# Performance work log

Hardware: AMD Instinct MI355X
Metric: run time of the kernel (lower is better)

Reference implementation:

```python
import jax, jax.numpy as jnp
import numpy as np

B, T, IN, H, OUT = 256, 100, 128, 1024, 35
BITS = 4
SLOPE = 25.0
THR_H = 1.0
THR_O = 1.0
BETA1, BETA2, BETA3, BETA4 = 0.9, 0.85, 0.8, 0.95


def fake_quant(w, w_min, w_max, bits=BITS):
    # FakeQuantize in training mode: STE -> forward value is quantized, grad passes through clamp
    levels = 2 ** bits
    scale = (w_max - w_min) / (levels - 1)
    wc = jnp.clip(w, w_min, w_max)
    q = jnp.round((wc - w_min) / scale) * scale + w_min
    return wc + jax.lax.stop_gradient(q - wc)


@jax.custom_vjp
def spike(x):
    # Heaviside forward, fast-sigmoid surrogate backward (snn.surrogate.fast_sigmoid)
    return (x > 0).astype(x.dtype)

def _spike_fwd(x):
    return (x > 0).astype(x.dtype), x

def _spike_bwd(x, g):
    return (g / (SLOPE * jnp.abs(x) + 1.0) ** 2,)

spike.defvjp(_spike_fwd, _spike_bwd)


def lif_step(cur, mem, beta, thr, reset_mechanism):
    # snntorch Leaky (reset_delay semantics): reset computed from previous mem, detached
    reset = jax.lax.stop_gradient((mem > thr).astype(cur.dtype))
    base = beta * mem + cur
    if reset_mechanism == "subtract":
        mem_new = base - reset * thr
    else:  # "zero"
        mem_new = base - reset * base
    spk = spike(mem_new - thr)
    return spk, mem_new


def setup_inputs() -> dict:
    key = jax.random.key(0)
    ks = jax.random.split(key, 5)
    x = jax.random.normal(ks[0], (B, T, IN), dtype=jnp.float32)
    # QuantLinear init: uniform(w_min, w_max); fc1 uses (-0.5, 0.5), others (0.001, 1.0)
    w1 = jax.random.uniform(ks[1], (H, IN), minval=-0.5, maxval=0.5, dtype=jnp.float32)
    w2 = jax.random.uniform(ks[2], (H, H), minval=0.001, maxval=1.0, dtype=jnp.float32)
    w3 = jax.random.uniform(ks[3], (H, H), minval=0.001, maxval=1.0, dtype=jnp.float32)
    w4 = jax.random.uniform(ks[4], (OUT, H), minval=0.001, maxval=1.0, dtype=jnp.float32)
    return {"x": x, "w1": w1, "w2": w2, "w3": w3, "w4": w4}


def reference(x, w1, w2, w3, w4):
    # hoist weight quantization out of the time loop (identical math each step)
    q1 = fake_quant(w1, -0.5, 0.5)
    q2 = fake_quant(w2, 0.001, 1.0)
    q3 = fake_quant(w3, 0.001, 1.0)
    q4 = fake_quant(w4, 0.001, 1.0)
    xs = jnp.transpose(x, (1, 0, 2)) / 15.0  # [T, B, IN]
    Bx = x.shape[0]

    def step(carry, xt):
        m1, m2, m3, m4 = carry
        s1, m1 = lif_step(xt @ q1.T, m1, BETA1, THR_H, "subtract")
        s2, m2 = lif_step(s1 @ q2.T, m2, BETA2, THR_H, "subtract")
        s3, m3 = lif_step(s2 @ q3.T, m3, BETA3, THR_H, "subtract")
        s4, m4 = lif_step(s3 @ q4.T, m4, BETA4, THR_O, "zero")
        return (m1, m2, m3, m4), (s1, s2, s3, s4, m4)

    init = (jnp.zeros((Bx, H), x.dtype), jnp.zeros((Bx, H), x.dtype),
            jnp.zeros((Bx, H), x.dtype), jnp.zeros((Bx, OUT), x.dtype))
    _, (spk1, spk2, spk3, spk4, mem4) = jax.lax.scan(step, init, xs)
    # stacked along time dim 0, matching torch.stack(dim=0)
    return spk1, spk2, spk3, spk4, mem4
```

## Files before the change

### kernel.cpp

```cpp
#include <hip/hip_runtime.h>
#include <stdint.h>

#define NB  256
#define NT  100
#define NIN 128
#define NH  1024
#define NOUT 35

#define O_SPK2 26214400ull
#define O_SPK3 52428800ull
#define O_SPK4 78643200ull
#define O_MEM4 79539200ull

#define WS_XT   0ull
#define WS_Q1T  13107200ull
#define WS_K2T  13631488ull
#define WS_K3T  14680064ull
#define WS_K4T  15728640ull

#define S2C ((float)((1.0 - 0.001) / 15.0))
#define S1C ((float)(1.0 / 15.0))

__global__ __launch_bounds__(256) void k_prep(const float* __restrict__ w1,
                       const float* __restrict__ w2, const float* __restrict__ w3,
                       const float* __restrict__ w4, uint8_t* __restrict__ ws)
{
  const int bid = blockIdx.x, tid = threadIdx.x;
  if (bid < 512) {
    const float* W = (bid < 256) ? w2 : w3;
    uint8_t* K = ws + ((bid < 256) ? WS_K2T : WS_K3T);
    const int tb = bid & 255;
    const int i0 = (tb & 15) << 6, j0 = (tb >> 4) << 6;
    __shared__ uint8_t tile[64 * 68];
    const int jl = tid >> 4, iq = (tid & 15) << 2;
    #pragma unroll
    for (int k = 0; k < 4; ++k) {
      const int jloc = jl + k * 16;
      const float4 v = *(const float4*)&W[(size_t)(j0 + jloc) * 1024 + i0 + iq];
      float wc;
      wc = fminf(fmaxf(v.x, 0.001f), 1.0f); tile[(iq + 0) * 68 + jloc] = (uint8_t)(int)rintf((wc - 0.001f) / S2C);
      wc = fminf(fmaxf(v.y, 0.001f), 1.0f); tile[(iq + 1) * 68 + jloc] = (uint8_t)(int)rintf((wc - 0.001f) / S2C);
      wc = fminf(fmaxf(v.z, 0.001f), 1.0f); tile[(iq + 2) * 68 + jloc] = (uint8_t)(int)rintf((wc - 0.001f) / S2C);
      wc = fminf(fmaxf(v.w, 0.001f), 1.0f); tile[(iq + 3) * 68 + jloc] = (uint8_t)(int)rintf((wc - 0.001f) / S2C);
    }
    __syncthreads();
    const int li = tid >> 2, cq = tid & 3;
    const uint32_t* tp = (const uint32_t*)&tile[li * 68 + (cq << 4)];
    *(uint4*)&K[(size_t)(i0 + li) * 1024 + j0 + (cq << 4)] =
        make_uint4(tp[0], tp[1], tp[2], tp[3]);
    return;
  }
  long long id = (long long)(bid - 512) * 256 + tid;
  if (id < 49152) {
    int i = (int)(id / 48), j = (int)(id % 48);
    uint8_t v = 0;
    if (j < NOUT) {
      float wv = w4[(size_t)j * 1024 + i];
      float wc = fminf(fmaxf(wv, 0.001f), 1.0f);
      v = (uint8_t)(int)rintf((wc - 0.001f) / S2C);
    }
    ws[WS_K4T + id] = v;
    return;
  }
  id -= 49152;
  if (id < 131072) {
    int i = (int)(id >> 10), j = (int)(id & 1023);
    float wv = w1[(size_t)j * 128 + i];
    float wc = fminf(fmaxf(wv, -0.5f), 0.5f);
    float q = rintf((wc + 0.5f) / S1C) * S1C - 0.5f;
    ((float*)(ws + WS_Q1T))[id] = q;
  }
}

__global__ __launch_bounds__(512, 1) void k_spk1(const float* __restrict__ x,
                                                 const float* __restrict__ q1T,
                                                 float* __restrict__ out)
{
  const int b = blockIdx.x;
  const int tid = threadIdx.x;
  const int lane = tid & 63;
  const float* xb = x + (size_t)b * NT * NIN;
  float m1a = 0.f, m1b = 0.f;

  for (int c = 0; c < 4; ++c) {
    float xv0[25], xv1[25];
    #pragma unroll
    for (int tt = 0; tt < 25; ++tt) {
      const float* xr = xb + (size_t)(c * 25 + tt) * NIN;
      xv0[tt] = xr[lane] / 15.0f;
      xv1[tt] = xr[lane + 64] / 15.0f;
    }
    float acc0[25], acc1[25];
    #pragma unroll
    for (int tt = 0; tt < 25; ++tt) { acc0[tt] = 0.f; acc1[tt] = 0.f; }

    #pragma unroll 2
    for (int ib = 0; ib < 8; ++ib) {
      float q0[8], q1v[8];
      #pragma unroll
      for (int u = 0; u < 8; ++u) {
        q0[u]  = q1T[(size_t)(ib * 8 + u) * NH + tid];
        q1v[u] = q1T[(size_t)(ib * 8 + u) * NH + tid + 512];
      }
      #pragma unroll
      for (int tt = 0; tt < 25; ++tt) {
        #pragma unroll
        for (int u = 0; u < 8; ++u) {
          float xs = __int_as_float(__builtin_amdgcn_readlane(__float_as_int(xv0[tt]), ib * 8 + u));
          acc0[tt] = fmaf(xs, q0[u], acc0[tt]);
          acc1[tt] = fmaf(xs, q1v[u], acc1[tt]);
        }
      }
    }
    #pragma unroll 2
    for (int ib = 8; ib < 16; ++ib) {
      float q0[8], q1v[8];
      #pragma unroll
      for (int u = 0; u < 8; ++u) {
        q0[u]  = q1T[(size_t)(ib * 8 + u) * NH + tid];
        q1v[u] = q1T[(size_t)(ib * 8 + u) * NH + tid + 512];
      }
      #pragma unroll
      for (int tt = 0; tt < 25; ++tt) {
        #pragma unroll
        for (int u = 0; u < 8; ++u) {
          float xs = __int_as_float(__builtin_amdgcn_readlane(__float_as_int(xv1[tt]), ib * 8 + u - 64));
          acc0[tt] = fmaf(xs, q0[u], acc0[tt]);
          acc1[tt] = fmaf(xs, q1v[u], acc1[tt]);
        }
      }
    }
    #pragma unroll
    for (int tt = 0; tt < 25; ++tt) {
      const int t = c * 25 + tt;
      const size_t row = ((size_t)t * NB + b) * (size_t)NH;
      float rst0 = m1a > 1.0f ? 1.0f : 0.0f;
      m1a = fmaf(0.9f, m1a, acc0[tt]) - rst0;
      out[row + tid] = ((m1a - 1.0f) > 0.0f) ? 1.0f : 0.0f;
      float rst1 = m1b > 1.0f ? 1.0f : 0.0f;
      m1b = fmaf(0.9f, m1b, acc1[tt]) - rst1;
      out[row + tid + 512] = ((m1b - 1.0f) > 0.0f) ? 1.0f : 0.0f;
    }
  }
}

#define ACC(V) do { \
  aE0 += (V).x & 0x00FF00FFu; aO0 += ((V).x >> 8) & 0x00FF00FFu; \
  aE1 += (V).y & 0x00FF00FFu; aO1 += ((V).y >> 8) & 0x00FF00FFu; \
  aE2 += (V).z & 0x00FF00FFu; aO2 += ((V).z >> 8) & 0x00FF00FFu; \
  aE3 += (V).w & 0x00FF00FFu; aO3 += ((V).w >> 8) & 0x00FF00FFu; } while (0)

__global__ __launch_bounds__(1024, 1) void k_main(
    const uint8_t* __restrict__ k2T, const uint8_t* __restrict__ k3T,
    const uint8_t* __restrict__ k4T, float* __restrict__ out)
{
  const int b = blockIdx.x;
  const int tid = threadIdx.x;
  const int lane = tid & 63;
  const int wave = tid >> 6;

  __shared__ uint16_t list[1024];
  __shared__ uint4    pEa4[1024];
  __shared__ uint4    pOa4[1024];
  __shared__ uint4    wcnt4[4];
  uint32_t* pEa  = (uint32_t*)pEa4;
  uint32_t* pOa  = (uint32_t*)pOa4;
  uint32_t* wcnt = (uint32_t*)wcnt4;

  float m2 = 0.f, m3 = 0.f, m4 = 0.f;
  uint32_t nT, nL; bool cm;

  auto buildList = [&](uint64_t bal) {
    const uint4 c0 = wcnt4[0], c1 = wcnt4[1], c2 = wcnt4[2], c3 = wcnt4[3];
    nT = c0.x + c0.y + c0.z + c0.w + c1.x + c1.y + c1.z + c1.w +
         c2.x + c2.y + c2.z + c2.w + c3.x + c3.y + c3.z + c3.w;
    cm = nT > 512;
    nL = cm ? (1024u - nT) : nT;
    uint32_t pre = 0;
    const int w = wave;
    pre += (w > 0)  ? c0.x : 0u;  pre += (w > 1)  ? c0.y : 0u;
    pre += (w > 2)  ? c0.z : 0u;  pre += (w > 3)  ? c0.w : 0u;
    pre += (w > 4)  ? c1.x : 0u;  pre += (w > 5)  ? c1.y : 0u;
    pre += (w > 6)  ? c1.z : 0u;  pre += (w > 7)  ? c1.w : 0u;
    pre += (w > 8)  ? c2.x : 0u;  pre += (w > 9)  ? c2.y : 0u;
    pre += (w > 10) ? c2.z : 0u;  pre += (w > 11) ? c2.w : 0u;
    pre += (w > 12) ? c3.x : 0u;  pre += (w > 13) ? c3.y : 0u;
    pre += (w > 14) ? c3.z : 0u;
    const uint32_t bs = cm ? ((uint32_t)(w << 6) - pre) : pre;
    const uint64_t cw = cm ? ~bal : bal;
    if ((cw >> lane) & 1ull)
      list[bs + (uint32_t)__popcll(cw & ((1ull << lane) - 1ull))] = (uint16_t)tid;
  };

  auto gatherBig = [&](const uint8_t* __restrict__ mat, uint32_t nLv) {
    uint32_t aE0=0,aE1=0,aE2=0,aE3=0,aO0=0,aO1=0,aO2=0,aO3=0;
    const uint8_t* bp = mat + (lane << 4);
    uint32_t a = (uint32_t)wave;
    for (; a + 48 < nLv; a += 64) {
      uint32_t i0 = (uint32_t)__builtin_amdgcn_readfirstlane((int)list[a]);
      uint32_t i1 = (uint32_t)__builtin_amdgcn_readfirstlane((int)list[a + 16]);
      uint32_t i2 = (uint32_t)__builtin_amdgcn_readfirstlane((int)list[a + 32]);
      uint32_t i3 = (uint32_t)__builtin_amdgcn_readfirstlane((int)list[a + 48]);
      const uint4 v0 = *(const uint4*)(bp + ((size_t)i0 << 10));
      const uint4 v1 = *(const uint4*)(bp + ((size_t)i1 << 10));
      const uint4 v2 = *(const uint4*)(bp + ((size_t)i2 << 10));
      const uint4 v3 = *(const uint4*)(bp + ((size_t)i3 << 10));
      ACC(v0); ACC(v1); ACC(v2); ACC(v3);
    }
    for (; a < nLv; a += 16) {
      uint32_t i0 = (uint32_t)__builtin_amdgcn_readfirstlane((int)list[a]);
      const uint4 v0 = *(const uint4*)(bp + ((size_t)i0 << 10));
      ACC(v0);
    }
    const int basei = (wave << 8) + (lane << 2);
    *(uint4*)&pEa[basei] = make_uint4(aE0, aE1, aE2, aE3);
    *(uint4*)&pOa[basei] = make_uint4(aO0, aO1, aO2, aO3);
  };

  auto gatherAll = [&](const uint8_t* __restrict__ mat) {
    uint32_t aE0=0,aE1=0,aE2=0,aE3=0,aO0=0,aO1=0,aO2=0,aO3=0;
    const uint8_t* bp = mat + (lane << 4);
    for (uint32_t a = (uint32_t)wave; a + 48 < 1024u; a += 64) {
      const uint4 v0 = *(const uint4*)(bp + ((size_t)a << 10));
      const uint4 v1 = *(const uint4*)(bp + ((size_t)(a + 16) << 10));
      const uint4 v2 = *(const uint4*)(bp + ((size_t)(a + 32) << 10));
      const uint4 v3 = *(const uint4*)(bp + ((size_t)(a + 48) << 10));
      ACC(v0); ACC(v1); ACC(v2); ACC(v3);
    }
    const int basei = (wave << 8) + (lane << 2);
    *(uint4*)&pEa[basei] = make_uint4(aE0, aE1, aE2, aE3);
    *(uint4*)&pOa[basei] = make_uint4(aO0, aO1, aO2, aO3);
  };

  auto gather4 = [&](uint32_t nLv) {
    uint32_t aE0=0,aE1=0,aE2=0,aE3=0,aO0=0,aO1=0,aO2=0,aO3=0;
    const uint8_t* bp = k4T + (lane << 4);
    uint32_t a = (uint32_t)wave;
    for (; a + 48 < nLv; a += 64) {
      uint32_t i0 = (uint32_t)__builtin_amdgcn_readfirstlane((int)list[a]);
      uint32_t i1 = (uint32_t)__builtin_amdgcn_readfirstlane((int)list[a + 16]);
      uint32_t i2 = (uint32_t)__builtin_amdgcn_readfirstlane((int)list[a + 32]);
      uint32_t i3 = (uint32_t)__builtin_amdgcn_readfirstlane((int)list[a + 48]);
      const uint4 v0 = *(const uint4*)(bp + (size_t)i0 * 48u);
      const uint4 v1 = *(const uint4*)(bp + (size_t)i1 * 48u);
      const uint4 v2 = *(const uint4*)(bp + (size_t)i2 * 48u);
      const uint4 v3 = *(const uint4*)(bp + (size_t)i3 * 48u);
      ACC(v0); ACC(v1); ACC(v2); ACC(v3);
    }
    for (; a < nLv; a += 16) {
      uint32_t i0 = (uint32_t)__builtin_amdgcn_readfirstlane((int)list[a]);
      const uint4 v0 = *(const uint4*)(bp + (size_t)i0 * 48u);
      ACC(v0);
    }
    const int basei = (wave << 8) + (lane << 2);
    *(uint4*)&pEa[basei] = make_uint4(aE0, aE1, aE2, aE3);
    *(uint4*)&pOa[basei] = make_uint4(aO0, aO1, aO2, aO3);
  };

  auto gather4All = [&]() {
    uint32_t aE0=0,aE1=0,aE2=0,aE3=0,aO0=0,aO1=0,aO2=0,aO3=0;
    const uint8_t* bp = k4T + (lane << 4);
    for (uint32_t a = (uint32_t)wave; a + 48 < 1024u; a += 64) {
      const uint4 v0 = *(const uint4*)(bp + (size_t)a * 48u);
      const uint4 v1 = *(const uint4*)(bp + (size_t)(a + 16) * 48u);
      const uint4 v2 = *(const uint4*)(bp + (size_t)(a + 32) * 48u);
      const uint4 v3 = *(const uint4*)(bp + (size_t)(a + 48) * 48u);
      ACC(v0); ACC(v1); ACC(v2); ACC(v3);
    }
    const int basei = (wave << 8) + (lane << 2);
    *(uint4*)&pEa[basei] = make_uint4(aE0, aE1, aE2, aE3);
    *(uint4*)&pOa[basei] = make_uint4(aO0, aO1, aO2, aO3);
  };

  auto gsum = [&](int jn) -> uint32_t {
    const int w = jn >> 2, sh = (jn & 2) << 3;
    const uint32_t* P = (jn & 1) ? pOa : pEa;
    uint32_t s = 0;
    #pragma unroll
    for (int g = 0; g < 16; ++g) s += P[(g << 8) + w];
    return (s >> sh) & 0xffffu;
  };

  gatherAll(k2T);
  __syncthreads();
  const uint32_t r2v = gsum(tid);
  __syncthreads();
  gatherAll(k3T);
  __syncthreads();
  const uint32_t r3v = gsum(tid);
  __syncthreads();
  if (lane < 3) gather4All();
  __syncthreads();
  const uint32_t r4v = (tid < NOUT) ? gsum(tid) : 0u;

  float s1v = out[(size_t)b * NH + tid];

  for (int t = 0; t < NT; ++t) {
    const size_t rowH = ((size_t)t * NB + b) * (size_t)NH;
    const size_t rowO = ((size_t)t * NB + b) * (size_t)NOUT;

    bool sA = s1v > 0.5f;
    {
      int tn = (t + 1 < NT) ? (t + 1) : t;
      s1v = out[((size_t)tn * NB + b) * (size_t)NH + tid];
    }
    uint64_t b1 = __ballot(sA);
    if (lane == 0) wcnt[wave] = (uint32_t)__popcll(b1);
    __syncthreads();
    buildList(b1);
    __syncthreads();
    const uint32_t n1 = nT, nl1 = nL; const bool cm1 = cm;
    if (nl1) gatherBig(k2T, nl1);
    __syncthreads();

    bool sp;
    {
      uint32_t gsv = nl1 ? gsum(tid) : 0u;
      uint32_t K = cm1 ? (r2v - gsv) : gsv;
      float cur = fmaf(S2C, (float)K, 0.001f * (float)n1);
      float rst = m2 > 1.0f ? 1.0f : 0.0f;
      m2 = fmaf(0.85f, m2, cur) - rst;
      sp = (m2 - 1.0f) > 0.0f;
      out[O_SPK2 + rowH + tid] = sp ? 1.0f : 0.0f;
    }
    uint64_t b2 = __ballot(sp);
    if (lane == 0) wcnt[wave] = (uint32_t)__popcll(b2);
    __syncthreads();
    buildList(b2);
    __syncthreads();
    const uint32_t n2 = nT, nl2 = nL; const bool cm2 = cm;
    if (nl2) gatherBig(k3T, nl2);
    __syncthreads();

    {
      uint32_t gsv = nl2 ? gsum(tid) : 0u;
      uint32_t K = cm2 ? (r3v - gsv) : gsv;
      float cur = fmaf(S2C, (float)K, 0.001f * (float)n2);
      float rst = m3 > 1.0f ? 1.0f : 0.0f;
      m3 = fmaf(0.8f, m3, cur) - rst;
      sp = (m3 - 1.0f) > 0.0f;
      out[O_SPK3 + rowH + tid] = sp ? 1.0f : 0.0f;
    }
    uint64_t b3 = __ballot(sp);
    if (lane == 0) wcnt[wave] = (uint32_t)__popcll(b3);
    __syncthreads();
    buildList(b3);
    __syncthreads();
    const uint32_t n3 = nT, nl3 = nL; const bool cm3 = cm;

    if (nl3 && lane < 3) gather4(nl3);
    __syncthreads();

    if (tid < NOUT) {
      uint32_t gsv = nl3 ? gsum(tid) : 0u;
      uint32_t K = cm3 ? (r4v - gsv) : gsv;
      float cur = fmaf(S2C, (float)K, 0.001f * (float)n3);
      float rst = m4 > 1.0f ? 1.0f : 0.0f;
      float bsv = fmaf(0.95f, m4, cur);
      m4 = (rst > 0.0f) ? 0.0f : bsv;
      out[O_SPK4 + rowO + tid] = ((m4 - 1.0f) > 0.0f) ? 1.0f : 0.0f;
      out[O_MEM4 + rowO + tid] = m4;
    }
  }
}
#undef ACC

extern "C" void kernel_launch(void* const* d_in, const int* in_sizes, int n_in,
                              void* d_out, int out_size, void* d_ws, size_t ws_size,
                              hipStream_t stream)
{
  const float* x  = (const float*)d_in[0];
  const float* w1 = (const float*)d_in[1];
  const float* w2 = (const float*)d_in[2];
  const float* w3 = (const float*)d_in[3];
  const float* w4 = (const float*)d_in[4];
  float* out = (float*)d_out;
  uint8_t* ws = (uint8_t*)d_ws;
  hipLaunchKernelGGL(k_prep, dim3(1216), dim3(256), 0, stream, w1, w2, w3, w4, ws);
  hipLaunchKernelGGL(k_spk1, dim3(256),  dim3(512), 0, stream,
                     x, (const float*)(ws + WS_Q1T), out);
  hipLaunchKernelGGL(k_main, dim3(256),  dim3(1024), 0, stream,
                     ws + WS_K2T, ws + WS_K3T, ws + WS_K4T, out);
}
```

Baseline: 743.7 us.

## Pre-transpose x in prep, vectorize layer-1 GEMM, use LDS-only barriers

```diff
diff --git a/kernel.cpp b/kernel.cpp
--- a/kernel.cpp
+++ b/kernel.cpp
@@ -21,7 +21,14 @@
 #define S2C ((float)((1.0 - 0.001) / 15.0))
 #define S1C ((float)(1.0 / 15.0))
 
-__global__ __launch_bounds__(256) void k_prep(const float* __restrict__ w1,
+#define BARRIER() do { \
+  asm volatile("s_waitcnt lgkmcnt(0)" ::: "memory"); \
+  __builtin_amdgcn_s_barrier(); \
+  asm volatile("" ::: "memory"); \
+} while (0)
+
+__global__ __launch_bounds__(256) void k_prep(const float* __restrict__ x,
+                       const float* __restrict__ w1,
                        const float* __restrict__ w2, const float* __restrict__ w3,
                        const float* __restrict__ w4, uint8_t* __restrict__ ws)
 {
@@ -68,65 +75,48 @@
     float wv = w1[(size_t)j * 128 + i];
     float wc = fminf(fmaxf(wv, -0.5f), 0.5f);
     float q = rintf((wc + 0.5f) / S1C) * S1C - 0.5f;
-    ((float*)(ws + WS_Q1T))[id] = q;
+    ((float*)(ws + WS_Q1T))[(size_t)i * 1024 + ((j & 255) << 2) + (j >> 8)] = q;
+    return;
+  }
+  id -= 131072;
+  if (id < 3276800) {
+    int row = (int)(id >> 7), i = (int)(id & 127);
+    int tt = row >> 8, bb = row & 255;
+    ((float*)(ws + WS_XT))[id] = x[((size_t)bb * NT + tt) * NIN + i] / 15.0f;
   }
 }
 
-__global__ __launch_bounds__(512, 1) void k_spk1(const float* __restrict__ x,
-                                                 const float* __restrict__ q1T,
+__global__ __launch_bounds__(256, 1) void k_spk1(const float* __restrict__ xt,
+                                                 const float* __restrict__ q1X,
                                                  float* __restrict__ out)
 {
   const int b = blockIdx.x;
   const int tid = threadIdx.x;
-  const int lane = tid & 63;
-  const float* xb = x + (size_t)b * NT * NIN;
-  float m1a = 0.f, m1b = 0.f;
+  float m[4] = {0.f, 0.f, 0.f, 0.f};
 
   for (int c = 0; c < 4; ++c) {
-    float xv0[25], xv1[25];
+    float acc[4][25];
     #pragma unroll
     for (int tt = 0; tt < 25; ++tt) {
-      const float* xr = xb + (size_t)(c * 25 + tt) * NIN;
-      xv0[tt] = xr[lane] / 15.0f;
-      xv1[tt] = xr[lane + 64] / 15.0f;
-    }
-    float acc0[25], acc1[25];
-    #pragma unroll
-    for (int tt = 0; tt < 25; ++tt) { acc0[tt] = 0.f; acc1[tt] = 0.f; }
-
-    #pragma unroll 2
-    for (int ib = 0; ib < 8; ++ib) {
-      float q0[8], q1v[8];
+      acc[0][tt] = 0.f; acc[1][tt] = 0.f; acc[2][tt] = 0.f; acc[3][tt] = 0.f;
+    }
+    for (int ib = 0; ib < 16; ++ib) {
+      float4 q[8];
       #pragma unroll
-      for (int u = 0; u < 8; ++u) {
-        q0[u]  = q1T[(size_t)(ib * 8 + u) * NH + tid];
-        q1v[u] = q1T[(size_t)(ib * 8 + u) * NH + tid + 512];
-      }
+      for (int u = 0; u < 8; ++u)
+        q[u] = *(const float4*)&q1X[(size_t)(ib * 8 + u) * 1024 + (tid << 2)];
       #pragma unroll
       for (int tt = 0; tt < 25; ++tt) {
+        const float* xr = xt + ((size_t)(c * 25 + tt) * NB + b) * NIN + ib * 8;
+        const float4 xa = *(const float4*)xr;
+        const float4 xc = *(const float4*)(xr + 4);
+        float xs[8] = {xa.x, xa.y, xa.z, xa.w, xc.x, xc.y, xc.z, xc.w};
         #pragma unroll
         for (int u = 0; u < 8; ++u) {
-          float xs = __int_as_float(__builtin_amdgcn_readlane(__float_as_int(xv0[tt]), ib * 8 + u));
-          acc0[tt] = fmaf(xs, q0[u], acc0[tt]);
-          acc1[tt] = fmaf(xs, q1v[u], acc1[tt]);
-        }
-      }
-    }
-    #pragma unroll 2
-    for (int ib = 8; ib < 16; ++ib) {
-      float q0[8], q1v[8];
-      #pragma unroll
-      for (int u = 0; u < 8; ++u) {
-        q0[u]  = q1T[(size_t)(ib * 8 + u) * NH + tid];
-        q1v[u] = q1T[(size_t)(ib * 8 + u) * NH + tid + 512];
-      }
-      #pragma unroll
-      for (int tt = 0; tt < 25; ++tt) {
-        #pragma unroll
-        for (int u = 0; u < 8; ++u) {
-          float xs = __int_as_float(__builtin_amdgcn_readlane(__float_as_int(xv1[tt]), ib * 8 + u - 64));
-          acc0[tt] = fmaf(xs, q0[u], acc0[tt]);
-          acc1[tt] = fmaf(xs, q1v[u], acc1[tt]);
+          acc[0][tt] = fmaf(xs[u], q[u].x, acc[0][tt]);
+          acc[1][tt] = fmaf(xs[u], q[u].y, acc[1][tt]);
+          acc[2][tt] = fmaf(xs[u], q[u].z, acc[2][tt]);
+          acc[3][tt] = fmaf(xs[u], q[u].w, acc[3][tt]);
         }
       }
     }
@@ -134,12 +124,12 @@
     for (int tt = 0; tt < 25; ++tt) {
       const int t = c * 25 + tt;
       const size_t row = ((size_t)t * NB + b) * (size_t)NH;
-      float rst0 = m1a > 1.0f ? 1.0f : 0.0f;
-      m1a = fmaf(0.9f, m1a, acc0[tt]) - rst0;
-      out[row + tid] = ((m1a - 1.0f) > 0.0f) ? 1.0f : 0.0f;
-      float rst1 = m1b > 1.0f ? 1.0f : 0.0f;
-      m1b = fmaf(0.9f, m1b, acc1[tt]) - rst1;
-      out[row + tid + 512] = ((m1b - 1.0f) > 0.0f) ? 1.0f : 0.0f;
+      #pragma unroll
+      for (int n = 0; n < 4; ++n) {
+        float rst = m[n] > 1.0f ? 1.0f : 0.0f;
+        m[n] = fmaf(0.9f, m[n], acc[n][tt]) - rst;
+        out[row + n * 256 + tid] = ((m[n] - 1.0f) > 0.0f) ? 1.0f : 0.0f;
+      }
     }
   }
 }
@@ -282,15 +272,15 @@
   };
 
   gatherAll(k2T);
-  __syncthreads();
+  BARRIER();
   const uint32_t r2v = gsum(tid);
-  __syncthreads();
+  BARRIER();
   gatherAll(k3T);
-  __syncthreads();
+  BARRIER();
   const uint32_t r3v = gsum(tid);
-  __syncthreads();
+  BARRIER();
   if (lane < 3) gather4All();
-  __syncthreads();
+  BARRIER();
   const uint32_t r4v = (tid < NOUT) ? gsum(tid) : 0u;
 
   float s1v = out[(size_t)b * NH + tid];
@@ -306,12 +296,12 @@
     }
     uint64_t b1 = __ballot(sA);
     if (lane == 0) wcnt[wave] = (uint32_t)__popcll(b1);
-    __syncthreads();
+    BARRIER();
     buildList(b1);
-    __syncthreads();
+    BARRIER();
     const uint32_t n1 = nT, nl1 = nL; const bool cm1 = cm;
     if (nl1) gatherBig(k2T, nl1);
-    __syncthreads();
+    BARRIER();
 
     bool sp;
     {
@@ -325,12 +315,12 @@
     }
     uint64_t b2 = __ballot(sp);
     if (lane == 0) wcnt[wave] = (uint32_t)__popcll(b2);
-    __syncthreads();
+    BARRIER();
     buildList(b2);
-    __syncthreads();
+    BARRIER();
     const uint32_t n2 = nT, nl2 = nL; const bool cm2 = cm;
     if (nl2) gatherBig(k3T, nl2);
-    __syncthreads();
+    BARRIER();
 
     {
       uint32_t gsv = nl2 ? gsum(tid) : 0u;
@@ -343,13 +333,13 @@
     }
     uint64_t b3 = __ballot(sp);
     if (lane == 0) wcnt[wave] = (uint32_t)__popcll(b3);
-    __syncthreads();
+    BARRIER();
     buildList(b3);
-    __syncthreads();
+    BARRIER();
     const uint32_t n3 = nT, nl3 = nL; const bool cm3 = cm;
 
     if (nl3 && lane < 3) gather4(nl3);
-    __syncthreads();
+    BARRIER();
 
     if (tid < NOUT) {
       uint32_t gsv = nl3 ? gsum(tid) : 0u;
@@ -376,9 +366,9 @@
   const float* w4 = (const float*)d_in[4];
   float* out = (float*)d_out;
   uint8_t* ws = (uint8_t*)d_ws;
-  hipLaunchKernelGGL(k_prep, dim3(1216), dim3(256), 0, stream, w1, w2, w3, w4, ws);
-  hipLaunchKernelGGL(k_spk1, dim3(256),  dim3(512), 0, stream,
-                     x, (const float*)(ws + WS_Q1T), out);
+  hipLaunchKernelGGL(k_prep, dim3(14016), dim3(256), 0, stream, x, w1, w2, w3, w4, ws);
+  hipLaunchKernelGGL(k_spk1, dim3(256),  dim3(256), 0, stream,
+                     (const float*)(ws + WS_XT), (const float*)(ws + WS_Q1T), out);
   hipLaunchKernelGGL(k_main, dim3(256),  dim3(1024), 0, stream,
                      ws + WS_K2T, ws + WS_K3T, ws + WS_K4T, out);
 }
```

Result: slower. 878.0 us (+18.1%).
